# Performance work log

Measured on AMD Instinct MI355X. Metric: run time of the kernel, lower is better.

## Reference

```python
import jax, jax.numpy as jnp
import numpy as np
from jax import lax

B, T_IN, D = 32, 512, 384
F = 384      # x_predictor_filter_size
K = 3        # kernel, padding=1 -> same length
LN_EPS = 1e-5


def setup_inputs() -> dict:
    key = jax.random.key(0)
    ks = jax.random.split(key, 8)
    s = 0.02
    return {
        "x": jax.random.normal(ks[0], (B, T_IN, D), dtype=jnp.float32),
        "target": jax.random.randint(ks[1], (B, T_IN), 0, 8, dtype=jnp.int32),
        "mel_max_length": 4096,
        "conv1_w": jax.random.normal(ks[2], (F, D, K), dtype=jnp.float32) * s,
        "conv1_b": jnp.zeros((F,), jnp.float32),
        "ln1_g": jnp.ones((F,), jnp.float32),
        "ln1_b": jnp.zeros((F,), jnp.float32),
        "conv2_w": jax.random.normal(ks[3], (F, F, K), dtype=jnp.float32) * s,
        "conv2_b": jnp.zeros((F,), jnp.float32),
        "ln2_g": jnp.ones((F,), jnp.float32),
        "ln2_b": jnp.zeros((F,), jnp.float32),
        "lin_w": jax.random.normal(ks[4], (F, 1), dtype=jnp.float32) * s,
        "lin_b": jnp.zeros((1,), jnp.float32),
    }


def _conv1d_same(h_ncl, w, b):
    # h_ncl: [B, C_in, T], w: [C_out, C_in, K], padding=1
    out = lax.conv_general_dilated(h_ncl, w, window_strides=(1,), padding=[(1, 1)],
                                   dimension_numbers=("NCH", "OIH", "NCH"))
    return out + b[None, :, None]


def _layernorm(h, g, b):
    mu = jnp.mean(h, axis=-1, keepdims=True)
    var = jnp.var(h, axis=-1, keepdims=True)
    return (h - mu) * lax.rsqrt(var + LN_EPS) * g + b


def _duration_predictor(x, conv1_w, conv1_b, ln1_g, ln1_b, conv2_w, conv2_b, ln2_g, ln2_b, lin_w, lin_b):
    h = _conv1d_same(jnp.transpose(x, (0, 2, 1)), conv1_w, conv1_b)       # [B,F,T]
    h = jax.nn.relu(_layernorm(jnp.transpose(h, (0, 2, 1)), ln1_g, ln1_b))  # [B,T,F]
    h = _conv1d_same(jnp.transpose(h, (0, 2, 1)), conv2_w, conv2_b)
    h = jax.nn.relu(_layernorm(jnp.transpose(h, (0, 2, 1)), ln2_g, ln2_b))
    return (h @ lin_w + lin_b)[..., 0]  # [B, T_in]


def _length_regulate(x, target, mel_max_length):
    # Equivalent to alignment @ x with one-hot alignment built by create_alignment,
    # expressed as a duration-indexed gather (same math, no dense [B,Tout,Tin]).
    ends = jnp.cumsum(target, axis=1)                 # [B, T_in]
    m = jnp.arange(mel_max_length)                    # [T_out]
    idx = jax.vmap(lambda e: jnp.searchsorted(e, m, side="right"))(ends)  # [B, T_out]
    valid = idx < target.shape[1]                     # frames past total duration -> zero pad
    idx = jnp.minimum(idx, target.shape[1] - 1)
    out = jnp.take_along_axis(x, idx[:, :, None], axis=1)  # [B, T_out, D]
    return out * valid[:, :, None].astype(x.dtype)


def reference(x, target, mel_max_length, conv1_w, conv1_b, ln1_g, ln1_b,
              conv2_w, conv2_b, ln2_g, ln2_b, lin_w, lin_b):
    dur_pred = _duration_predictor(x, conv1_w, conv1_b, ln1_g, ln1_b,
                                   conv2_w, conv2_b, ln2_g, ln2_b, lin_w, lin_b)
    output = _length_regulate(x, target, mel_max_length)
    return output, dur_pred
```

## Files before the change

### kernel.cpp

```cpp
#include <hip/hip_runtime.h>
#include <cstdint>
#include <cstddef>

#define B_   32
#define TIN  512
#define D_   384
#define F_   384
#define TOUT 4096

typedef __bf16 bf16x8 __attribute__((ext_vector_type(8)));
typedef float  f32x4  __attribute__((ext_vector_type(4)));
typedef unsigned short u16x8 __attribute__((ext_vector_type(8)));

__device__ __forceinline__ unsigned short f2bf(float f) {
  unsigned int u = __float_as_uint(f);
  u += 0x7fff + ((u >> 16) & 1);
  return (unsigned short)(u >> 16);
}

__device__ __forceinline__ void load16_to_lds(const void* g, void* l) {
  __builtin_amdgcn_global_load_lds(
      (const __attribute__((address_space(1))) unsigned int*)g,
      (__attribute__((address_space(3))) unsigned int*)l, 16, 0, 0);
}

#define PB_CUM 32
#define PB_W   1152
#define PB_TOT (PB_CUM + PB_W)

__global__ __launch_bounds__(256) void prep_all(
    const float* __restrict__ w1, const float* __restrict__ w2,
    unsigned short* __restrict__ Wt1, unsigned short* __restrict__ Wt2,
    const int* __restrict__ target, int* __restrict__ idxv) {
  int bx = blockIdx.x;
  int tid = threadIdx.x;

  if (bx < PB_CUM) {
    __shared__ int ends[512];
    __shared__ int ps[256];
    int b = bx;
    int a0 = target[b * TIN + 2 * tid];
    int a1 = target[b * TIN + 2 * tid + 1];
    ps[tid] = a0 + a1;
    __syncthreads();
    for (int off = 1; off < 256; off <<= 1) {
      int add = (tid >= off) ? ps[tid - off] : 0;
      __syncthreads();
      ps[tid] += add;
      __syncthreads();
    }
    int incl = ps[tid];
    ends[2 * tid + 1] = incl;
    ends[2 * tid]     = incl - a1;
    __syncthreads();
    for (int p = 0; p < 16; ++p) {
      int m = p * 256 + tid;
      int lo = 0, hi = 512;
      while (lo < hi) {
        int mid = (lo + hi) >> 1;
        if (ends[mid] <= m) lo = mid + 1; else hi = mid;
      }
      idxv[b * TOUT + m] = (lo < TIN) ? lo : -1;
    }
    return;
  }
  bx -= PB_CUM;

  {
    int g = bx * 256 + tid;
    const int FD = F_ * D_;
    int which = g >= FD;
    const float* w = which ? w2 : w1;
    unsigned short* o = which ? Wt2 : Wt1;
    int e = g - which * FD;
    o[e]          = f2bf(w[e * 3 + 0]);
    o[FD + e]     = f2bf(w[e * 3 + 1]);
    o[2 * FD + e] = f2bf(w[e * 3 + 2]);
  }
}

__global__ __launch_bounds__(512, 1) void mega(
    const unsigned short* __restrict__ Wt1, const unsigned short* __restrict__ Wt2,
    const float* __restrict__ b1, const float* __restrict__ g1, const float* __restrict__ be1,
    const float* __restrict__ b2, const float* __restrict__ g2, const float* __restrict__ be2,
    const float* __restrict__ lw, const float* __restrict__ lb,
    float* __restrict__ dur,
    const float4* __restrict__ x4, const int* __restrict__ idxv,
    float4* __restrict__ out4) {
  __shared__ __attribute__((aligned(16))) char smem[112128];
  char* As = smem;
  char* Bs = smem + 62976;

  const int bx  = blockIdx.x;
  const int tid = threadIdx.x;
  const int cb  = bx / 5;

  if (bx - cb * 5 != 0) {
    int gidx = bx - cb - 1;
    int b  = gidx >> 5;
    int r0 = (gidx & 31) * 128;
    const int* idxp = idxv + b * TOUT + r0;
    const f32x4* xb = (const f32x4*)(x4 + (size_t)b * (TIN * 96));
    f32x4* ob = (f32x4*)(out4 + ((size_t)b * TOUT + r0) * 96);
    #pragma unroll 8
    for (int it = 0; it < 24; ++it) {
      int j = it * 512 + tid;
      int row = j / 96;
      int c = j - row * 96;
      int id = idxp[row];
      f32x4 v = {0.f, 0.f, 0.f, 0.f};
      if (id >= 0) v = xb[id * 96 + c];
      __builtin_nontemporal_store(v, ob + j);
    }
    return;
  }

  const int wave = tid >> 6;
  const int lane = tid & 63;
  const int quad = lane >> 4;
  const int l15  = lane & 15;
  const int wn   = wave * 48;
  const int m0   = cb * 64;
  const int b    = m0 >> 9;
  const int t0   = m0 & 511;
  const int arow = tid >> 2;
  const int acol = (tid & 3) * 8;

  for (int p = 0; p < 7; ++p) {
    int ch = p * 512 + tid;
    if (ch < 3264) {
      int row = ch / 48;
      int ci  = ch - row * 48;
      int t   = t0 - 2 + row;
      u16x8 val;
      if ((unsigned)t >= (unsigned)TIN) {
        val = (u16x8)0;
      } else {
        const float4* xr = (const float4*)x4 + ((size_t)(b * TIN + t)) * 96 + ci * 2;
        float4 v0 = xr[0], v1 = xr[1];
        val[0] = f2bf(v0.x); val[1] = f2bf(v0.y); val[2] = f2bf(v0.z); val[3] = f2bf(v0.w);
        val[4] = f2bf(v1.x); val[5] = f2bf(v1.y); val[6] = f2bf(v1.z); val[7] = f2bf(v1.w);
      }
      unsigned int byte = ((unsigned int)(row * 768 + ci * 16)) ^ (((unsigned)row & 7u) << 4);
      *(u16x8*)(As + byte) = val;
    }
  }

  auto stageB = [&](const unsigned short* __restrict__ Wt, int kc, int buf) {
    int kw = kc / 12;
    int d0 = (kc - kw * 12) * 32;
    const unsigned short* src = Wt + (size_t)(kw * F_ + arow) * D_ + d0 + acol;
    char* dst = Bs + buf * 24576 + wave * 1024;
    for (int r = 0; r < 3; ++r)
      load16_to_lds(src + (size_t)(r * 128) * D_, dst + r * 8192);
  };

  f32x4 acc1[5][3];
  for (int i = 0; i < 5; ++i)
    for (int j = 0; j < 3; ++j)
      acc1[i][j] = (f32x4){0.f, 0.f, 0.f, 0.f};

  stageB(Wt1, 0, 0);
  __syncthreads();
  int cur = 0;
  #pragma unroll 1
  for (int kc = 0; kc < 36; ++kc) {
    if (kc < 35) stageB(Wt1, kc + 1, cur ^ 1);
    int kw = kc / 12;
    int d0 = (kc - kw * 12) * 32;
    const char* Bc = Bs + cur * 24576;
    bf16x8 bv[3];
    for (int ni = 0; ni < 3; ++ni)
      bv[ni] = *(const bf16x8*)(Bc + (wn + ni * 16 + l15) * 64 + quad * 16);
    int rb = l15 + kw;
    unsigned int sw = (((unsigned)rb) & 7u) << 4;
    unsigned int base = (unsigned int)(rb * 768 + d0 * 2 + quad * 16);
    bf16x8 av[5];
    for (int mi = 0; mi < 5; ++mi)
      av[mi] = *(const bf16x8*)(As + ((base + mi * 12288) ^ sw));
    for (int mi = 0; mi < 5; ++mi)
      for (int ni = 0; ni < 3; ++ni)
        acc1[mi][ni] = __builtin_amdgcn_mfma_f32_16x16x32_bf16(av[mi], bv[ni], acc1[mi][ni], 0, 0, 0);
    __syncthreads();
    cur ^= 1;
  }

  {
    float gv[6], bev[6];
    for (int j = 0; j < 6; ++j) {
      int c = lane + j * 64;
      gv[j] = g1[c]; bev[j] = be1[c];
    }
    float bb[3];
    for (int ni = 0; ni < 3; ++ni) bb[ni] = b1[wn + ni * 16 + l15];
    char* scr = Bs;

    for (int mi = 0; mi < 5; ++mi) {
      __syncthreads();
      for (int ni = 0; ni < 3; ++ni) {
        int cc = wn + ni * 16 + l15;
        for (int r = 0; r < 4; ++r) {
          int wr = quad * 4 + r;
          unsigned int byte = ((unsigned int)(wr * 1536 + cc * 4)) ^ ((((unsigned)wr >> 2) & 3u) << 4);
          *(float*)(scr + byte) = acc1[mi][ni][r] + bb[ni];
        }
      }
      __syncthreads();
      for (int rr = 0; rr < 2; ++rr) {
        int lr = wave * 2 + rr;
        int h = mi * 16 + lr;
        if (h >= 66) continue;
        unsigned int swr = ((((unsigned)lr) >> 2) & 3u) << 4;
        float v[6], s = 0.f, ss = 0.f;
        for (int j = 0; j < 6; ++j) {
          unsigned int byte = ((unsigned int)(lr * 1536 + (lane + j * 64) * 4)) ^ swr;
          v[j] = *(const float*)(scr + byte);
          s += v[j]; ss += v[j] * v[j];
        }
        for (int off = 32; off; off >>= 1) {
          s  += __shfl_xor(s, off);
          ss += __shfl_xor(ss, off);
        }
        float mean = s * (1.f / 384.f);
        float var  = ss * (1.f / 384.f) - mean * mean;
        float rstd = rsqrtf(var + 1e-5f);
        int th = t0 - 1 + h;
        bool valid = (unsigned)th < (unsigned)TIN;
        unsigned int hb = (((unsigned)h) & 7u) << 4;
        for (int j = 0; j < 6; ++j) {
          float y = (v[j] - mean) * rstd * gv[j] + bev[j];
          y = y > 0.f ? y : 0.f;
          if (!valid) y = 0.f;
          unsigned int byte = ((unsigned int)(h * 768 + (lane + j * 64) * 2)) ^ hb;
          *(unsigned short*)(As + byte) = f2bf(y);
        }
      }
    }
  }

  __syncthreads();
  f32x4 acc2[4][3];
  for (int i = 0; i < 4; ++i)
    for (int j = 0; j < 3; ++j)
      acc2[i][j] = (f32x4){0.f, 0.f, 0.f, 0.f};

  stageB(Wt2, 0, 0);
  __syncthreads();
  cur = 0;
  #pragma unroll 1
  for (int kc = 0; kc < 36; ++kc) {
    if (kc < 35) stageB(Wt2, kc + 1, cur ^ 1);
    int kw = kc / 12;
    int d0 = (kc - kw * 12) * 32;
    const char* Bc = Bs + cur * 24576;
    bf16x8 bv[3];
    for (int ni = 0; ni < 3; ++ni)
      bv[ni] = *(const bf16x8*)(Bc + (wn + ni * 16 + l15) * 64 + quad * 16);
    int rb = l15 + kw;
    unsigned int sw = (((unsigned)rb) & 7u) << 4;
    unsigned int base = (unsigned int)(rb * 768 + d0 * 2 + quad * 16);
    bf16x8 av[4];
    for (int mi = 0; mi < 4; ++mi)
      av[mi] = *(const bf16x8*)(As + ((base + mi * 12288) ^ sw));
    for (int mi = 0; mi < 4; ++mi)
      for (int ni = 0; ni < 3; ++ni)
        acc2[mi][ni] = __builtin_amdgcn_mfma_f32_16x16x32_bf16(av[mi], bv[ni], acc2[mi][ni], 0, 0, 0);
    __syncthreads();
    cur ^= 1;
  }

  {
    float gv[6], bev[6], lwv[6];
    for (int j = 0; j < 6; ++j) {
      int c = lane + j * 64;
      gv[j] = g2[c]; bev[j] = be2[c]; lwv[j] = lw[c];
    }
    float bb[3];
    for (int ni = 0; ni < 3; ++ni) bb[ni] = b2[wn + ni * 16 + l15];
    float lbv = lb[0];
    char* scr = Bs;

    for (int mi = 0; mi < 4; ++mi) {
      __syncthreads();
      for (int ni = 0; ni < 3; ++ni) {
        int cc = wn + ni * 16 + l15;
        for (int r = 0; r < 4; ++r) {
          int wr = quad * 4 + r;
          unsigned int byte = ((unsigned int)(wr * 1536 + cc * 4)) ^ ((((unsigned)wr >> 2) & 3u) << 4);
          *(float*)(scr + byte) = acc2[mi][ni][r] + bb[ni];
        }
      }
      __syncthreads();
      for (int rr = 0; rr < 2; ++rr) {
        int lr = wave * 2 + rr;
        int m = mi * 16 + lr;
        unsigned int swr = ((((unsigned)lr) >> 2) & 3u) << 4;
        float v[6], s = 0.f, ss = 0.f;
        for (int j = 0; j < 6; ++j) {
          unsigned int byte = ((unsigned int)(lr * 1536 + (lane + j * 64) * 4)) ^ swr;
          v[j] = *(const float*)(scr + byte);
          s += v[j]; ss += v[j] * v[j];
        }
        for (int off = 32; off; off >>= 1) {
          s  += __shfl_xor(s, off);
          ss += __shfl_xor(ss, off);
        }
        float mean = s * (1.f / 384.f);
        float var  = ss * (1.f / 384.f) - mean * mean;
        float rstd = rsqrtf(var + 1e-5f);
        float a = 0.f;
        for (int j = 0; j < 6; ++j) {
          float y = (v[j] - mean) * rstd * gv[j] + bev[j];
          y = y > 0.f ? y : 0.f;
          a += y * lwv[j];
        }
        for (int off = 32; off; off >>= 1) a += __shfl_xor(a, off);
        if (lane == 0) dur[m0 + m] = a + lbv;
      }
    }
  }
}

extern "C" void kernel_launch(void* const* d_in, const int* in_sizes, int n_in,
                              void* d_out, int out_size, void* d_ws, size_t ws_size,
                              hipStream_t stream) {
  const float* x      = (const float*)d_in[0];
  const int*   target = (const int*)d_in[1];
  const float* w1  = (const float*)d_in[3];
  const float* b1  = (const float*)d_in[4];
  const float* g1  = (const float*)d_in[5];
  const float* be1 = (const float*)d_in[6];
  const float* w2  = (const float*)d_in[7];
  const float* b2  = (const float*)d_in[8];
  const float* g2  = (const float*)d_in[9];
  const float* be2 = (const float*)d_in[10];
  const float* lw  = (const float*)d_in[11];
  const float* lb  = (const float*)d_in[12];

  float* out = (float*)d_out;
  float* dur = out + (size_t)B_ * TOUT * D_;

  char* ws = (char*)d_ws;
  unsigned short* Wt1  = (unsigned short*)(ws);
  unsigned short* Wt2  = (unsigned short*)(ws + 884736);
  int*            idxv = (int*)(ws + 1769472);

  prep_all<<<dim3(PB_TOT), dim3(256), 0, stream>>>(
      w1, w2, Wt1, Wt2, target, idxv);
  mega<<<dim3(1280), dim3(512), 0, stream>>>(
      Wt1, Wt2, b1, g1, be1, b2, g2, be2, lw, lb,
      dur, (const float4*)x, idxv, (float4*)out);
}
```

Measured before the change: 335.6 us.

## Move length-regulate gather into prep kernel, leaving conv kernel standalone

The output gather moves out of the big conv kernel, where it shared a grid with the conv blocks, into the first kernel alongside the weight conversion. Each of the 2048 gather blocks recomputes the prefix sum of its batch's durations and binary-searches only its 64 rows. This removes the global index buffer and the extra read of it. In exchange the memory-bound gather and the compute-bound conv no longer run concurrently, and the prefix-sum work is repeated 64 times per batch.

```diff
diff --git a/kernel.cpp b/kernel.cpp
--- a/kernel.cpp
+++ b/kernel.cpp
@@ -24,21 +24,22 @@
       (__attribute__((address_space(3))) unsigned int*)l, 16, 0, 0);
 }
 
-#define PB_CUM 32
-#define PB_W   1152
-#define PB_TOT (PB_CUM + PB_W)
-
-__global__ __launch_bounds__(256) void prep_all(
+#define GB 2048
+
+__global__ __launch_bounds__(256) void gather_prep(
     const float* __restrict__ w1, const float* __restrict__ w2,
     unsigned short* __restrict__ Wt1, unsigned short* __restrict__ Wt2,
-    const int* __restrict__ target, int* __restrict__ idxv) {
+    const int* __restrict__ target,
+    const f32x4* __restrict__ x4, f32x4* __restrict__ out4) {
   int bx = blockIdx.x;
   int tid = threadIdx.x;
 
-  if (bx < PB_CUM) {
+  if (bx < GB) {
     __shared__ int ends[512];
     __shared__ int ps[256];
-    int b = bx;
+    __shared__ int idx_s[64];
+    int b  = bx >> 6;
+    int r0 = (bx & 63) * 64;
     int a0 = target[b * TIN + 2 * tid];
     int a1 = target[b * TIN + 2 * tid + 1];
     ps[tid] = a0 + a1;
@@ -53,18 +54,31 @@
     ends[2 * tid + 1] = incl;
     ends[2 * tid]     = incl - a1;
     __syncthreads();
-    for (int p = 0; p < 16; ++p) {
-      int m = p * 256 + tid;
+    if (tid < 64) {
+      int m = r0 + tid;
       int lo = 0, hi = 512;
       while (lo < hi) {
         int mid = (lo + hi) >> 1;
         if (ends[mid] <= m) lo = mid + 1; else hi = mid;
       }
-      idxv[b * TOUT + m] = (lo < TIN) ? lo : -1;
+      idx_s[tid] = (lo < TIN) ? lo : -1;
+    }
+    __syncthreads();
+    const f32x4* xb = x4 + (size_t)b * (TIN * 96);
+    f32x4* ob = out4 + ((size_t)b * TOUT + r0) * 96;
+    #pragma unroll 4
+    for (int it = 0; it < 24; ++it) {
+      int j = it * 256 + tid;
+      int row = j / 96;
+      int c = j - row * 96;
+      int id = idx_s[row];
+      f32x4 v = {0.f, 0.f, 0.f, 0.f};
+      if (id >= 0) v = xb[id * 96 + c];
+      __builtin_nontemporal_store(v, ob + j);
     }
     return;
   }
-  bx -= PB_CUM;
+  bx -= GB;
 
   {
     int g = bx * 256 + tid;
@@ -79,41 +93,18 @@
   }
 }
 
-__global__ __launch_bounds__(512, 1) void mega(
+__global__ __launch_bounds__(512, 1) void conv(
     const unsigned short* __restrict__ Wt1, const unsigned short* __restrict__ Wt2,
     const float* __restrict__ b1, const float* __restrict__ g1, const float* __restrict__ be1,
     const float* __restrict__ b2, const float* __restrict__ g2, const float* __restrict__ be2,
     const float* __restrict__ lw, const float* __restrict__ lb,
-    float* __restrict__ dur,
-    const float4* __restrict__ x4, const int* __restrict__ idxv,
-    float4* __restrict__ out4) {
+    float* __restrict__ dur, const float4* __restrict__ x4) {
   __shared__ __attribute__((aligned(16))) char smem[112128];
   char* As = smem;
   char* Bs = smem + 62976;
 
-  const int bx  = blockIdx.x;
   const int tid = threadIdx.x;
-  const int cb  = bx / 5;
-
-  if (bx - cb * 5 != 0) {
-    int gidx = bx - cb - 1;
-    int b  = gidx >> 5;
-    int r0 = (gidx & 31) * 128;
-    const int* idxp = idxv + b * TOUT + r0;
-    const f32x4* xb = (const f32x4*)(x4 + (size_t)b * (TIN * 96));
-    f32x4* ob = (f32x4*)(out4 + ((size_t)b * TOUT + r0) * 96);
-    #pragma unroll 8
-    for (int it = 0; it < 24; ++it) {
-      int j = it * 512 + tid;
-      int row = j / 96;
-      int c = j - row * 96;
-      int id = idxp[row];
-      f32x4 v = {0.f, 0.f, 0.f, 0.f};
-      if (id >= 0) v = xb[id * 96 + c];
-      __builtin_nontemporal_store(v, ob + j);
-    }
-    return;
-  }
+  const int cb  = blockIdx.x;
 
   const int wave = tid >> 6;
   const int lane = tid & 63;
@@ -343,11 +334,9 @@
   char* ws = (char*)d_ws;
   unsigned short* Wt1  = (unsigned short*)(ws);
   unsigned short* Wt2  = (unsigned short*)(ws + 884736);
-  int*            idxv = (int*)(ws + 1769472);
-
-  prep_all<<<dim3(PB_TOT), dim3(256), 0, stream>>>(
-      w1, w2, Wt1, Wt2, target, idxv);
-  mega<<<dim3(1280), dim3(512), 0, stream>>>(
-      Wt1, Wt2, b1, g1, be1, b2, g2, be2, lw, lb,
-      dur, (const float4*)x, idxv, (float4*)out);
-}
+
+  gather_prep<<<dim3(GB + 1152), dim3(256), 0, stream>>>(
+      w1, w2, Wt1, Wt2, target, (const f32x4*)x, (f32x4*)out);
+  conv<<<dim3(256), dim3(512), 0, stream>>>(
+      Wt1, Wt2, b1, g1, be1, b2, g2, be2, lw, lb, dur, (const float4*)x);
+}
```

Result: no change. 331.1 us (-1.3%).
